# Kernel tuning notes

Measured on AMD Instinct MI355X. Metric: run time of the kernel, lower is better.

## Reference

```python
import jax, jax.numpy as jnp
import numpy as np

N_NODES = 50000
N_EDGES = 800000
IN_CH = 64
HID_CH = 64
OUT_CH = 64
NUM_GRAPHS = 256


def setup_inputs() -> dict:
    key = jax.random.key(0)
    ks = jax.random.split(key, 9)
    x = jax.random.normal(ks[0], (N_NODES, IN_CH), dtype=jnp.float32)
    edge_index = jax.random.randint(ks[1], (2, N_EDGES), 0, N_NODES, dtype=jnp.int64)
    batch = jnp.sort(jax.random.randint(ks[2], (N_NODES,), 0, NUM_GRAPHS, dtype=jnp.int64))
    def glorot(k, fan_in, fan_out):
        s = jnp.sqrt(6.0 / (fan_in + fan_out))
        return jax.random.uniform(k, (fan_in, fan_out), jnp.float32, -s, s)
    W1 = glorot(ks[3], IN_CH, HID_CH)
    b1 = jnp.zeros((HID_CH,), jnp.float32)
    W2 = glorot(ks[4], HID_CH, HID_CH)
    b2 = jnp.zeros((HID_CH,), jnp.float32)
    W3 = glorot(ks[5], HID_CH, OUT_CH)
    b3 = jnp.zeros((OUT_CH,), jnp.float32)
    return {"x": x, "edge_index": edge_index, "batch": batch,
            "W1": W1, "b1": b1, "W2": W2, "b2": b2, "W3": W3, "b3": b3}


def gcn_conv(x, src, dst, W, b):
    # PyG GCNConv: linear, add self-loops, symmetric deg normalization, scatter-add, bias
    n = x.shape[0]
    xw = x @ W                                   # [N, F_out]
    loops = jnp.arange(n, dtype=src.dtype)
    s = jnp.concatenate([src, loops])            # sources (with self loops)
    d = jnp.concatenate([dst, loops])            # targets (with self loops)
    ones = jnp.ones(d.shape, dtype=x.dtype)
    deg = jax.ops.segment_sum(ones, d, num_segments=n)
    dinv = jnp.where(deg > 0, jax.lax.rsqrt(deg), 0.0)
    norm = dinv[s] * dinv[d]                     # [E + N]
    msgs = norm[:, None] * xw[s]                 # gather + scale
    out = jax.ops.segment_sum(msgs, d, num_segments=n)
    return out + b


def reference(x, edge_index, batch, W1, b1, W2, b2, W3, b3):
    src, dst = edge_index[0], edge_index[1]
    h = jax.nn.relu(gcn_conv(x, src, dst, W1, b1))
    h = jax.nn.relu(gcn_conv(h, src, dst, W2, b2))
    h = gcn_conv(h, src, dst, W3, b3)
    # global_add_pool over graph ids
    pooled = jax.ops.segment_sum(h, batch, num_segments=NUM_GRAPHS)  # [G, OUT_CH]
    return pooled  # out_channels != 1, so no flatten
```

## Files before the change

### kernel.cpp

```cpp
#include <hip/hip_runtime.h>
#include <hip/hip_bf16.h>
#include <hip/hip_fp16.h>

#define N_NODES 50000
#define N_EDGES 800000
#define CH 64
#define N_GRAPHS 256
#define NBUCK 196
#define MAXB 4608
#define NPAD (NBUCK * MAXB)
#define CHUNK 2048
#define SCAT_BLK ((N_EDGES + CHUNK - 1) / CHUNK)
#define GEMM_BLK ((N_NODES + 31) / 32)

__device__ __forceinline__ unsigned bf16_rne(float f) {
    unsigned u = __float_as_uint(f);
    return (u + 0x7fffu + ((u >> 16) & 1u)) >> 16;
}
__device__ __forceinline__ float4 ldtab(const unsigned short* __restrict__ tab, int s, int c4) {
    uint2 u = *(const uint2*)(tab + ((size_t)s << 6) + c4);
    float4 r;
    r.x = __uint_as_float(u.x << 16);
    r.y = __uint_as_float(u.x & 0xffff0000u);
    r.z = __uint_as_float(u.y << 16);
    r.w = __uint_as_float(u.y & 0xffff0000u);
    return r;
}
__device__ __forceinline__ unsigned pack_sn(int s, float n) {
    return (unsigned)s | ((unsigned)__half_as_ushort(__float2half_rn(n)) << 16);
}
__device__ __forceinline__ float unpack_n(unsigned p) {
    return __half2float(__ushort_as_half((unsigned short)(p >> 16)));
}

__global__ void init_k(int* __restrict__ gcur, float* __restrict__ poolz) {
    int i = blockIdx.x * 256 + threadIdx.x;
    if (i < N_GRAPHS * CH + N_GRAPHS) poolz[i] = 0.0f;
    if (i < NBUCK) gcur[i] = i * MAXB;
}

union FusedSh {
    struct { float WT[64 * 68]; } g;
    struct {
        int hist[NBUCK]; int lofs[NBUCK]; int gbase[NBUCK]; int cur[NBUCK];
        int sc[256]; unsigned stage[CHUNK];
    } s;
};
__global__ __launch_bounds__(256) void gemm1_scatter(
        const float* __restrict__ x, const float* __restrict__ W1,
        unsigned short* __restrict__ xwout,
        const int* __restrict__ ei, int* __restrict__ gcur, unsigned* __restrict__ ebuf) {
    __shared__ FusedSh sh;
    int tid = threadIdx.x;
    if (blockIdx.x < SCAT_BLK) {
        for (int i = tid; i < NBUCK; i += 256) sh.s.hist[i] = 0;
        __syncthreads();
        int e0 = blockIdx.x * CHUNK;
        int n = min(CHUNK, N_EDGES - e0);
        int src[8], dst[8];
#pragma unroll
        for (int k = 0; k < 8; ++k) {
            int idx = k * 256 + tid;
            if (idx < n) {
                int e = e0 + idx;
                src[k] = ei[e];
                dst[k] = ei[N_EDGES + e];
                atomicAdd(&sh.s.hist[dst[k] >> 8], 1);
            } else dst[k] = -1;
        }
        __syncthreads();
        int v = (tid < NBUCK) ? sh.s.hist[tid] : 0;
        sh.s.sc[tid] = v;
        __syncthreads();
        for (int off = 1; off < 256; off <<= 1) {
            int t = (tid >= off) ? sh.s.sc[tid - off] : 0;
            __syncthreads();
            sh.s.sc[tid] += t;
            __syncthreads();
        }
        if (tid < NBUCK) {
            int ex = sh.s.sc[tid] - v;
            sh.s.lofs[tid] = ex;
            sh.s.cur[tid] = ex;
            sh.s.gbase[tid] = v ? atomicAdd(&gcur[tid], v) : 0;
        }
        __syncthreads();
#pragma unroll
        for (int k = 0; k < 8; ++k) {
            if (dst[k] >= 0) {
                int b = dst[k] >> 8;
                int p = atomicAdd(&sh.s.cur[b], 1);
                sh.s.stage[p] = (unsigned)src[k] | ((unsigned)(dst[k] & 255) << 16)
                                                | ((unsigned)b << 24);
            }
        }
        __syncthreads();
        for (int i = tid; i < n; i += 256) {
            unsigned p = sh.s.stage[i];
            int b = p >> 24;
            ebuf[sh.s.gbase[b] + (i - sh.s.lofs[b])] = p;
        }
    } else {
        for (int i = tid; i < 64 * 64; i += 256) {
            int k = i >> 6, c = i & 63;
            sh.g.WT[c * 68 + k] = W1[i];
        }
        __syncthreads();
        int lane = tid & 63;
        int wv = __builtin_amdgcn_readfirstlane(tid >> 6);
        int row0 = (blockIdx.x - SCAT_BLK) * 32 + wv * 8;
        if (row0 >= N_NODES) return;
        float acc[8] = {0.f, 0.f, 0.f, 0.f, 0.f, 0.f, 0.f, 0.f};
#pragma unroll 2
        for (int k = 0; k < 64; k += 4) {
            float4 w = *(const float4*)&sh.g.WT[lane * 68 + k];
#pragma unroll
            for (int r = 0; r < 8; ++r) {
                float4 xv = *(const float4*)&x[(size_t)(row0 + r) * 64 + k];
                acc[r] = fmaf(xv.x, w.x, acc[r]);
                acc[r] = fmaf(xv.y, w.y, acc[r]);
                acc[r] = fmaf(xv.z, w.z, acc[r]);
                acc[r] = fmaf(xv.w, w.w, acc[r]);
            }
        }
#pragma unroll
        for (int r = 0; r < 8; ++r)
            xwout[(size_t)(row0 + r) * 64 + lane] = (unsigned short)bf16_rne(acc[r]);
    }
}

__global__ void csr_bucket(const unsigned* __restrict__ ebuf, const int* __restrict__ gcur,
                           int* __restrict__ deg, int* __restrict__ rowp,
                           float* __restrict__ dinv, int* __restrict__ col) {
    __shared__ int nd[256];
    __shared__ int cur[256];
    __shared__ int sc[256];
    int b = blockIdx.x;
    int tid = threadIdx.x;
    nd[tid] = 0;
    __syncthreads();
    int es = b * MAXB, ee = gcur[b];
    for (int e = es + tid; e < ee; e += 256)
        atomicAdd(&nd[(ebuf[e] >> 16) & 255], 1);
    __syncthreads();
    int v = nd[tid];
    sc[tid] = v;
    __syncthreads();
    for (int off = 1; off < 256; off <<= 1) {
        int t = (tid >= off) ? sc[tid - off] : 0;
        __syncthreads();
        sc[tid] += t;
        __syncthreads();
    }
    int node = b * 256 + tid;
    int lstart = es + sc[tid] - v;
    if (node < N_NODES) {
        deg[node] = v;
        rowp[node] = lstart;
        dinv[node] = rsqrtf((float)v + 1.0f);
    }
    cur[tid] = lstart;
    __syncthreads();
    for (int e = es + tid; e < ee; e += 256) {
        unsigned p = ebuf[e];
        int pos = atomicAdd(&cur[(p >> 16) & 255], 1);
        col[pos] = (int)(p & 0xFFFFu);
    }
}

__global__ void gemm_reg_bf16(const unsigned short* __restrict__ in,
                              const float* __restrict__ W,
                              unsigned short* __restrict__ out, int n) {
    __shared__ float WT[64 * 68];
    int tid = threadIdx.x;
    for (int i = tid; i < 64 * 64; i += 256) {
        int k = i >> 6, c = i & 63;
        WT[c * 68 + k] = W[i];
    }
    __syncthreads();
    int lane = tid & 63;
    int wv = __builtin_amdgcn_readfirstlane(tid >> 6);
    int row0 = blockIdx.x * 32 + wv * 8;
    if (row0 >= n) return;
    float acc[8] = {0.f, 0.f, 0.f, 0.f, 0.f, 0.f, 0.f, 0.f};
#pragma unroll 2
    for (int k = 0; k < 64; k += 8) {
        float4 w0 = *(const float4*)&WT[lane * 68 + k];
        float4 w1 = *(const float4*)&WT[lane * 68 + k + 4];
#pragma unroll
        for (int r = 0; r < 8; ++r) {
            uint4 xb = *(const uint4*)&in[(size_t)(row0 + r) * 64 + k];
            acc[r] = fmaf(__uint_as_float(xb.x << 16),         w0.x, acc[r]);
            acc[r] = fmaf(__uint_as_float(xb.x & 0xffff0000u), w0.y, acc[r]);
            acc[r] = fmaf(__uint_as_float(xb.y << 16),         w0.z, acc[r]);
            acc[r] = fmaf(__uint_as_float(xb.y & 0xffff0000u), w0.w, acc[r]);
            acc[r] = fmaf(__uint_as_float(xb.z << 16),         w1.x, acc[r]);
            acc[r] = fmaf(__uint_as_float(xb.z & 0xffff0000u), w1.y, acc[r]);
            acc[r] = fmaf(__uint_as_float(xb.w << 16),         w1.z, acc[r]);
            acc[r] = fmaf(__uint_as_float(xb.w & 0xffff0000u), w1.w, acc[r]);
        }
    }
#pragma unroll
    for (int r = 0; r < 8; ++r)
        out[(size_t)(row0 + r) * 64 + lane] = (unsigned short)bf16_rne(acc[r]);
}

template <int USE_PCK, int WRITE_PCK>
__global__ void agg_v4(const int* __restrict__ rowp, const int* __restrict__ deg,
                       const int* __restrict__ col, const float* __restrict__ dinv,
                       unsigned* __restrict__ pck,
                       const unsigned short* __restrict__ tab, const float* __restrict__ bias,
                       unsigned short* __restrict__ outv, int do_relu) {
    int wv = __builtin_amdgcn_readfirstlane(threadIdx.x >> 6);
    int node = blockIdx.x * 4 + wv;
    int lane = threadIdx.x & 63;
    int q = lane >> 4;
    int c4 = (lane & 15) << 2;
    float dd = dinv[node];
    int cnt = deg[node];
    int start = rowp[node];
    float4 acc = make_float4(0.f, 0.f, 0.f, 0.f);
    if (q == 0) {
        float4 xs = ldtab(tab, node, c4);
        float dd2 = dd * dd;
        acc.x = xs.x * dd2; acc.y = xs.y * dd2; acc.z = xs.z * dd2; acc.w = xs.w * dd2;
    }
    int j = 0;
    for (; j + 16 <= cnt; j += 16) {
        int s[4]; float nv[4];
#pragma unroll
        for (int u = 0; u < 4; ++u) {
            int idx = start + j + 4 * u + q;
            if (USE_PCK) {
                unsigned p = pck[idx];
                s[u] = (int)(p & 0xFFFFu);
                nv[u] = unpack_n(p);
            } else {
                s[u] = col[idx];
                nv[u] = dinv[s[u]] * dd;
                if (WRITE_PCK && (lane & 15) == 0) pck[idx] = pack_sn(s[u], nv[u]);
            }
        }
#pragma unroll
        for (int u = 0; u < 4; ++u) {
            float4 xv = ldtab(tab, s[u], c4);
            acc.x = fmaf(nv[u], xv.x, acc.x); acc.y = fmaf(nv[u], xv.y, acc.y);
            acc.z = fmaf(nv[u], xv.z, acc.z); acc.w = fmaf(nv[u], xv.w, acc.w);
        }
    }
    for (; j + 8 <= cnt; j += 8) {
        int s[2]; float nv[2];
#pragma unroll
        for (int u = 0; u < 2; ++u) {
            int idx = start + j + 4 * u + q;
            if (USE_PCK) {
                unsigned p = pck[idx];
                s[u] = (int)(p & 0xFFFFu);
                nv[u] = unpack_n(p);
            } else {
                s[u] = col[idx];
                nv[u] = dinv[s[u]] * dd;
                if (WRITE_PCK && (lane & 15) == 0) pck[idx] = pack_sn(s[u], nv[u]);
            }
        }
#pragma unroll
        for (int u = 0; u < 2; ++u) {
            float4 xv = ldtab(tab, s[u], c4);
            acc.x = fmaf(nv[u], xv.x, acc.x); acc.y = fmaf(nv[u], xv.y, acc.y);
            acc.z = fmaf(nv[u], xv.z, acc.z); acc.w = fmaf(nv[u], xv.w, acc.w);
        }
    }
    for (; j < cnt; j += 4) {
        int jj = j + q;
        bool valid = jj < cnt;
        int s; float nv;
        if (USE_PCK) {
            unsigned p = pck[start + (valid ? jj : 0)];
            s = (int)(p & 0xFFFFu);
            nv = valid ? unpack_n(p) : 0.0f;
        } else {
            s = col[start + (valid ? jj : 0)];
            nv = valid ? dinv[s] * dd : 0.0f;
            if (WRITE_PCK && valid && (lane & 15) == 0) pck[start + jj] = pack_sn(s, nv);
        }
        float4 xv = ldtab(tab, s, c4);
        acc.x = fmaf(nv, xv.x, acc.x); acc.y = fmaf(nv, xv.y, acc.y);
        acc.z = fmaf(nv, xv.z, acc.z); acc.w = fmaf(nv, xv.w, acc.w);
    }
    acc.x += __shfl_xor(acc.x, 16); acc.y += __shfl_xor(acc.y, 16);
    acc.z += __shfl_xor(acc.z, 16); acc.w += __shfl_xor(acc.w, 16);
    acc.x += __shfl_xor(acc.x, 32); acc.y += __shfl_xor(acc.y, 32);
    acc.z += __shfl_xor(acc.z, 32); acc.w += __shfl_xor(acc.w, 32);
    if (q == 0) {
        if (bias) {
            float4 bv = *(const float4*)&bias[c4];
            acc.x += bv.x; acc.y += bv.y; acc.z += bv.z; acc.w += bv.w;
        }
        if (do_relu) {
            acc.x = fmaxf(acc.x, 0.f); acc.y = fmaxf(acc.y, 0.f);
            acc.z = fmaxf(acc.z, 0.f); acc.w = fmaxf(acc.w, 0.f);
        }
        uint2 o;
        o.x = bf16_rne(acc.x) | (bf16_rne(acc.y) << 16);
        o.y = bf16_rne(acc.z) | (bf16_rne(acc.w) << 16);
        *(uint2*)&outv[((size_t)node << 6) + c4] = o;
    }
}

__global__ void pool_seg(const unsigned short* __restrict__ h, const int* __restrict__ batch,
                         float* __restrict__ pool, float* __restrict__ cntg) {
    int ch = threadIdx.x & 63;
    int grp = threadIdx.x >> 6;
    int base = (blockIdx.x * 4 + grp) * 16;
    float acc = 0.0f;
    int curg = -1, runlen = 0;
    for (int n = 0; n < 16; ++n) {
        int node = base + n;
        if (node >= N_NODES) break;
        int g = batch[node];
        float v = __uint_as_float(((unsigned)h[((size_t)node << 6) + ch]) << 16);
        if (g != curg) {
            if (curg >= 0) {
                atomicAdd(&pool[curg * 64 + ch], acc);
                if (ch == 0) atomicAdd(&cntg[curg], (float)runlen);
            }
            curg = g; acc = v; runlen = 1;
        } else { acc += v; runlen++; }
    }
    if (curg >= 0) {
        atomicAdd(&pool[curg * 64 + ch], acc);
        if (ch == 0) atomicAdd(&cntg[curg], (float)runlen);
    }
}

__global__ void out_gemm(const float* __restrict__ P, const float* __restrict__ cntg,
                         const float* __restrict__ W, const float* __restrict__ b,
                         float* __restrict__ out) {
    __shared__ float Ws[64 * 64];
    int tid = threadIdx.x;
    for (int i = tid; i < 64 * 64; i += 256) Ws[i] = W[i];
    __syncthreads();
    int lane = tid & 63;
    int g = blockIdx.x * 4 + (tid >> 6);
    if (g >= N_GRAPHS) return;
    float pv = P[g * 64 + lane];
    float acc = 0.0f;
#pragma unroll
    for (int k = 0; k < 64; ++k)
        acc = fmaf(__shfl(pv, k, 64), Ws[k * 64 + lane], acc);
    out[g * 64 + lane] = acc + cntg[g] * b[lane];
}

extern "C" void kernel_launch(void* const* d_in, const int* in_sizes, int n_in,
                              void* d_out, int out_size, void* d_ws, size_t ws_size,
                              hipStream_t stream) {
    const float* x   = (const float*)d_in[0];
    const int* ei    = (const int*)d_in[1];
    const int* batch = (const int*)d_in[2];
    const float* W1  = (const float*)d_in[3];
    const float* b1  = (const float*)d_in[4];
    const float* W2  = (const float*)d_in[5];
    const float* b2  = (const float*)d_in[6];
    const float* W3  = (const float*)d_in[7];
    const float* b3  = (const float*)d_in[8];
    float* out = (float*)d_out;

    char* ws = (char*)d_ws;
    float*    dinv = (float*)(ws);
    int*      DEG  = (int*)(ws + 200192);
    int*      ROWP = (int*)(ws + 400384);
    int*      COL  = (int*)(ws + 600576);
    unsigned* PCK  = (unsigned*)(ws + 4213248);
    float*    XW   = (float*)(ws + 7825920);
    float*    ACC  = (float*)(ws + 20625920);
    float*    POOL = (float*)(ws + 33425920);
    float*    CNT  = (float*)(ws + 33491456);
    int*      GCUR = (int*)(ws + 33492480);
    unsigned* EBUF = (unsigned*)(ws + 33493504);

    const int WAVE_NODE_BLK = N_NODES / 4;

    init_k<<<66, 256, 0, stream>>>(GCUR, POOL);

    gemm1_scatter<<<SCAT_BLK + GEMM_BLK, 256, 0, stream>>>(
        x, W1, (unsigned short*)XW, ei, GCUR, EBUF);

    csr_bucket<<<NBUCK, 256, 0, stream>>>(EBUF, GCUR, DEG, ROWP, dinv, COL);

    agg_v4<0, 1><<<WAVE_NODE_BLK, 256, 0, stream>>>(ROWP, DEG, COL, dinv, PCK,
        (const unsigned short*)XW, b1, (unsigned short*)ACC, 1);

    gemm_reg_bf16<<<GEMM_BLK, 256, 0, stream>>>((const unsigned short*)ACC, W2,
        (unsigned short*)XW, N_NODES);
    agg_v4<1, 0><<<WAVE_NODE_BLK, 256, 0, stream>>>(ROWP, DEG, COL, dinv, PCK,
        (const unsigned short*)XW, b2, (unsigned short*)ACC, 1);

    agg_v4<1, 0><<<WAVE_NODE_BLK, 256, 0, stream>>>(ROWP, DEG, COL, dinv, PCK,
        (const unsigned short*)ACC, nullptr, (unsigned short*)XW, 0);
    pool_seg<<<(N_NODES + 63) / 64, 256, 0, stream>>>((const unsigned short*)XW,
        batch, POOL, CNT);
    out_gemm<<<N_GRAPHS / 4, 256, 0, stream>>>(POOL, CNT, W3, b3, out);
}
```

Measured before the change: 231.4 us.

## Fuse layer-1 aggregation with layer-2 GEMM and fold pool zeroing into CSR build

The first aggregation kernel now also applies bias and ReLU and multiplies each node row by W2 in-register, using wave shuffles and W2 held in shared memory. This removes the separate gemm_reg_bf16 launch and the round trip of the intermediate activation through global memory. Zeroing of the pool buffer moves from init_k into csr_bucket, so init_k shrinks to one block. The fused kernel adds a 16 KB shared-memory W2 load per 4-node block and extra shuffles, which may lower occupancy and add per-block overhead.

```diff
diff --git a/kernel.cpp b/kernel.cpp
--- a/kernel.cpp
+++ b/kernel.cpp
@@ -33,10 +33,8 @@
     return __half2float(__ushort_as_half((unsigned short)(p >> 16)));
 }
 
-__global__ void init_k(int* __restrict__ gcur, float* __restrict__ poolz) {
-    int i = blockIdx.x * 256 + threadIdx.x;
-    if (i < N_GRAPHS * CH + N_GRAPHS) poolz[i] = 0.0f;
-    if (i < NBUCK) gcur[i] = i * MAXB;
+__global__ void init_k(int* __restrict__ gcur) {
+    if (threadIdx.x < NBUCK) gcur[threadIdx.x] = threadIdx.x * MAXB;
 }
 
 union FusedSh {
@@ -131,12 +129,17 @@
 
 __global__ void csr_bucket(const unsigned* __restrict__ ebuf, const int* __restrict__ gcur,
                            int* __restrict__ deg, int* __restrict__ rowp,
-                           float* __restrict__ dinv, int* __restrict__ col) {
+                           float* __restrict__ dinv, int* __restrict__ col,
+                           float* __restrict__ poolz) {
     __shared__ int nd[256];
     __shared__ int cur[256];
     __shared__ int sc[256];
     int b = blockIdx.x;
     int tid = threadIdx.x;
+    {
+        int zi = b * 85 + (tid % 85);
+        if (tid < 85 && zi < N_GRAPHS * CH + N_GRAPHS) poolz[zi] = 0.0f;
+    }
     nd[tid] = 0;
     __syncthreads();
     int es = b * MAXB, ee = gcur[b];
@@ -168,47 +171,113 @@
     }
 }
 
-__global__ void gemm_reg_bf16(const unsigned short* __restrict__ in,
-                              const float* __restrict__ W,
-                              unsigned short* __restrict__ out, int n) {
-    __shared__ float WT[64 * 68];
+__global__ void agg1_gemm2(const int* __restrict__ rowp, const int* __restrict__ deg,
+                           const int* __restrict__ col, const float* __restrict__ dinv,
+                           unsigned* __restrict__ pck,
+                           const unsigned short* __restrict__ tab,
+                           const float* __restrict__ b1, const float* __restrict__ W2,
+                           unsigned short* __restrict__ xw2out) {
+    __shared__ float Wsh[64 * 64];
     int tid = threadIdx.x;
-    for (int i = tid; i < 64 * 64; i += 256) {
-        int k = i >> 6, c = i & 63;
-        WT[c * 68 + k] = W[i];
-    }
-    __syncthreads();
+    for (int i = tid; i < 64 * 64; i += 256) Wsh[i] = W2[i];
+    __syncthreads();
+    int wv = __builtin_amdgcn_readfirstlane(tid >> 6);
+    int node = blockIdx.x * 4 + wv;
     int lane = tid & 63;
-    int wv = __builtin_amdgcn_readfirstlane(tid >> 6);
-    int row0 = blockIdx.x * 32 + wv * 8;
-    if (row0 >= n) return;
-    float acc[8] = {0.f, 0.f, 0.f, 0.f, 0.f, 0.f, 0.f, 0.f};
-#pragma unroll 2
-    for (int k = 0; k < 64; k += 8) {
-        float4 w0 = *(const float4*)&WT[lane * 68 + k];
-        float4 w1 = *(const float4*)&WT[lane * 68 + k + 4];
-#pragma unroll
-        for (int r = 0; r < 8; ++r) {
-            uint4 xb = *(const uint4*)&in[(size_t)(row0 + r) * 64 + k];
-            acc[r] = fmaf(__uint_as_float(xb.x << 16),         w0.x, acc[r]);
-            acc[r] = fmaf(__uint_as_float(xb.x & 0xffff0000u), w0.y, acc[r]);
-            acc[r] = fmaf(__uint_as_float(xb.y << 16),         w0.z, acc[r]);
-            acc[r] = fmaf(__uint_as_float(xb.y & 0xffff0000u), w0.w, acc[r]);
-            acc[r] = fmaf(__uint_as_float(xb.z << 16),         w1.x, acc[r]);
-            acc[r] = fmaf(__uint_as_float(xb.z & 0xffff0000u), w1.y, acc[r]);
-            acc[r] = fmaf(__uint_as_float(xb.w << 16),         w1.z, acc[r]);
-            acc[r] = fmaf(__uint_as_float(xb.w & 0xffff0000u), w1.w, acc[r]);
-        }
-    }
-#pragma unroll
-    for (int r = 0; r < 8; ++r)
-        out[(size_t)(row0 + r) * 64 + lane] = (unsigned short)bf16_rne(acc[r]);
-}
-
-template <int USE_PCK, int WRITE_PCK>
+    int q = lane >> 4;
+    int c4 = (lane & 15) << 2;
+    float dd = dinv[node];
+    int cnt = deg[node];
+    int start = rowp[node];
+    float4 acc = make_float4(0.f, 0.f, 0.f, 0.f);
+    if (q == 0) {
+        float4 xs = ldtab(tab, node, c4);
+        float dd2 = dd * dd;
+        acc.x = xs.x * dd2; acc.y = xs.y * dd2; acc.z = xs.z * dd2; acc.w = xs.w * dd2;
+    }
+    int j = 0;
+    for (; j + 16 <= cnt; j += 16) {
+        int s[4]; float nv[4];
+#pragma unroll
+        for (int u = 0; u < 4; ++u) {
+            int idx = start + j + 4 * u + q;
+            s[u] = col[idx];
+            nv[u] = dinv[s[u]] * dd;
+            if ((lane & 15) == 0) pck[idx] = pack_sn(s[u], nv[u]);
+        }
+#pragma unroll
+        for (int u = 0; u < 4; ++u) {
+            float4 xv = ldtab(tab, s[u], c4);
+            acc.x = fmaf(nv[u], xv.x, acc.x); acc.y = fmaf(nv[u], xv.y, acc.y);
+            acc.z = fmaf(nv[u], xv.z, acc.z); acc.w = fmaf(nv[u], xv.w, acc.w);
+        }
+    }
+    for (; j + 8 <= cnt; j += 8) {
+        int s[2]; float nv[2];
+#pragma unroll
+        for (int u = 0; u < 2; ++u) {
+            int idx = start + j + 4 * u + q;
+            s[u] = col[idx];
+            nv[u] = dinv[s[u]] * dd;
+            if ((lane & 15) == 0) pck[idx] = pack_sn(s[u], nv[u]);
+        }
+#pragma unroll
+        for (int u = 0; u < 2; ++u) {
+            float4 xv = ldtab(tab, s[u], c4);
+            acc.x = fmaf(nv[u], xv.x, acc.x); acc.y = fmaf(nv[u], xv.y, acc.y);
+            acc.z = fmaf(nv[u], xv.z, acc.z); acc.w = fmaf(nv[u], xv.w, acc.w);
+        }
+    }
+    for (; j < cnt; j += 4) {
+        int jj = j + q;
+        bool valid = jj < cnt;
+        int s = col[start + (valid ? jj : 0)];
+        float nv = valid ? dinv[s] * dd : 0.0f;
+        if (valid && (lane & 15) == 0) pck[start + jj] = pack_sn(s, nv);
+        float4 xv = ldtab(tab, s, c4);
+        acc.x = fmaf(nv, xv.x, acc.x); acc.y = fmaf(nv, xv.y, acc.y);
+        acc.z = fmaf(nv, xv.z, acc.z); acc.w = fmaf(nv, xv.w, acc.w);
+    }
+    acc.x += __shfl_xor(acc.x, 16); acc.y += __shfl_xor(acc.y, 16);
+    acc.z += __shfl_xor(acc.z, 16); acc.w += __shfl_xor(acc.w, 16);
+    acc.x += __shfl_xor(acc.x, 32); acc.y += __shfl_xor(acc.y, 32);
+    acc.z += __shfl_xor(acc.z, 32); acc.w += __shfl_xor(acc.w, 32);
+    {
+        float4 bv = *(const float4*)&b1[c4];
+        acc.x = fmaxf(acc.x + bv.x, 0.f); acc.y = fmaxf(acc.y + bv.y, 0.f);
+        acc.z = fmaxf(acc.z + bv.z, 0.f); acc.w = fmaxf(acc.w + bv.w, 0.f);
+    }
+    float hq[16];
+#pragma unroll
+    for (int t = 0; t < 4; ++t) {
+        int sl = 4 * q + t;
+        hq[4 * t + 0] = __shfl(acc.x, sl, 64);
+        hq[4 * t + 1] = __shfl(acc.y, sl, 64);
+        hq[4 * t + 2] = __shfl(acc.z, sl, 64);
+        hq[4 * t + 3] = __shfl(acc.w, sl, 64);
+    }
+    float4 g = make_float4(0.f, 0.f, 0.f, 0.f);
+#pragma unroll
+    for (int kk = 0; kk < 16; ++kk) {
+        int k = 16 * q + kk;
+        float4 wv = *(const float4*)&Wsh[(k << 6) + c4];
+        g.x = fmaf(hq[kk], wv.x, g.x); g.y = fmaf(hq[kk], wv.y, g.y);
+        g.z = fmaf(hq[kk], wv.z, g.z); g.w = fmaf(hq[kk], wv.w, g.w);
+    }
+    g.x += __shfl_xor(g.x, 16); g.y += __shfl_xor(g.y, 16);
+    g.z += __shfl_xor(g.z, 16); g.w += __shfl_xor(g.w, 16);
+    g.x += __shfl_xor(g.x, 32); g.y += __shfl_xor(g.y, 32);
+    g.z += __shfl_xor(g.z, 32); g.w += __shfl_xor(g.w, 32);
+    if (q == 0) {
+        uint2 o;
+        o.x = bf16_rne(g.x) | (bf16_rne(g.y) << 16);
+        o.y = bf16_rne(g.z) | (bf16_rne(g.w) << 16);
+        *(uint2*)&xw2out[((size_t)node << 6) + c4] = o;
+    }
+}
+
 __global__ void agg_v4(const int* __restrict__ rowp, const int* __restrict__ deg,
-                       const int* __restrict__ col, const float* __restrict__ dinv,
-                       unsigned* __restrict__ pck,
+                       const float* __restrict__ dinv, const unsigned* __restrict__ pck,
                        const unsigned short* __restrict__ tab, const float* __restrict__ bias,
                        unsigned short* __restrict__ outv, int do_relu) {
     int wv = __builtin_amdgcn_readfirstlane(threadIdx.x >> 6);
@@ -230,16 +299,9 @@
         int s[4]; float nv[4];
 #pragma unroll
         for (int u = 0; u < 4; ++u) {
-            int idx = start + j + 4 * u + q;
-            if (USE_PCK) {
-                unsigned p = pck[idx];
-                s[u] = (int)(p & 0xFFFFu);
-                nv[u] = unpack_n(p);
-            } else {
-                s[u] = col[idx];
-                nv[u] = dinv[s[u]] * dd;
-                if (WRITE_PCK && (lane & 15) == 0) pck[idx] = pack_sn(s[u], nv[u]);
-            }
+            unsigned p = pck[start + j + 4 * u + q];
+            s[u] = (int)(p & 0xFFFFu);
+            nv[u] = unpack_n(p);
         }
 #pragma unroll
         for (int u = 0; u < 4; ++u) {
@@ -252,16 +314,9 @@
         int s[2]; float nv[2];
 #pragma unroll
         for (int u = 0; u < 2; ++u) {
-            int idx = start + j + 4 * u + q;
-            if (USE_PCK) {
-                unsigned p = pck[idx];
-                s[u] = (int)(p & 0xFFFFu);
-                nv[u] = unpack_n(p);
-            } else {
-                s[u] = col[idx];
-                nv[u] = dinv[s[u]] * dd;
-                if (WRITE_PCK && (lane & 15) == 0) pck[idx] = pack_sn(s[u], nv[u]);
-            }
+            unsigned p = pck[start + j + 4 * u + q];
+            s[u] = (int)(p & 0xFFFFu);
+            nv[u] = unpack_n(p);
         }
 #pragma unroll
         for (int u = 0; u < 2; ++u) {
@@ -273,16 +328,9 @@
     for (; j < cnt; j += 4) {
         int jj = j + q;
         bool valid = jj < cnt;
-        int s; float nv;
-        if (USE_PCK) {
-            unsigned p = pck[start + (valid ? jj : 0)];
-            s = (int)(p & 0xFFFFu);
-            nv = valid ? unpack_n(p) : 0.0f;
-        } else {
-            s = col[start + (valid ? jj : 0)];
-            nv = valid ? dinv[s] * dd : 0.0f;
-            if (WRITE_PCK && valid && (lane & 15) == 0) pck[start + jj] = pack_sn(s, nv);
-        }
+        unsigned p = pck[start + (valid ? jj : 0)];
+        int s = (int)(p & 0xFFFFu);
+        float nv = valid ? unpack_n(p) : 0.0f;
         float4 xv = ldtab(tab, s, c4);
         acc.x = fmaf(nv, xv.x, acc.x); acc.y = fmaf(nv, xv.y, acc.y);
         acc.z = fmaf(nv, xv.z, acc.z); acc.w = fmaf(nv, xv.w, acc.w);
@@ -380,24 +428,22 @@
 
     const int WAVE_NODE_BLK = N_NODES / 4;
 
-    init_k<<<66, 256, 0, stream>>>(GCUR, POOL);
+    init_k<<<1, 256, 0, stream>>>(GCUR);
 
     gemm1_scatter<<<SCAT_BLK + GEMM_BLK, 256, 0, stream>>>(
         x, W1, (unsigned short*)XW, ei, GCUR, EBUF);
 
-    csr_bucket<<<NBUCK, 256, 0, stream>>>(EBUF, GCUR, DEG, ROWP, dinv, COL);
-
-    agg_v4<0, 1><<<WAVE_NODE_BLK, 256, 0, stream>>>(ROWP, DEG, COL, dinv, PCK,
-        (const unsigned short*)XW, b1, (unsigned short*)ACC, 1);
-
-    gemm_reg_bf16<<<GEMM_BLK, 256, 0, stream>>>((const unsigned short*)ACC, W2,
-        (unsigned short*)XW, N_NODES);
-    agg_v4<1, 0><<<WAVE_NODE_BLK, 256, 0, stream>>>(ROWP, DEG, COL, dinv, PCK,
-        (const unsigned short*)XW, b2, (unsigned short*)ACC, 1);
-
-    agg_v4<1, 0><<<WAVE_NODE_BLK, 256, 0, stream>>>(ROWP, DEG, COL, dinv, PCK,
-        (const unsigned short*)ACC, nullptr, (unsigned short*)XW, 0);
-    pool_seg<<<(N_NODES + 63) / 64, 256, 0, stream>>>((const unsigned short*)XW,
+    csr_bucket<<<NBUCK, 256, 0, stream>>>(EBUF, GCUR, DEG, ROWP, dinv, COL, POOL);
+
+    agg1_gemm2<<<WAVE_NODE_BLK, 256, 0, stream>>>(ROWP, DEG, COL, dinv, PCK,
+        (const unsigned short*)XW, b1, W2, (unsigned short*)ACC);
+
+    agg_v4<<<WAVE_NODE_BLK, 256, 0, stream>>>(ROWP, DEG, dinv, PCK,
+        (const unsigned short*)ACC, b2, (unsigned short*)XW, 1);
+
+    agg_v4<<<WAVE_NODE_BLK, 256, 0, stream>>>(ROWP, DEG, dinv, PCK,
+        (const unsigned short*)XW, nullptr, (unsigned short*)ACC, 0);
+    pool_seg<<<(N_NODES + 63) / 64, 256, 0, stream>>>((const unsigned short*)ACC,
         batch, POOL, CNT);
     out_gemm<<<N_GRAPHS / 4, 256, 0, stream>>>(POOL, CNT, W3, b3, out);
 }
```

New measurement: 227.0 us. No clear change (-1.9%).
